# Performance work log

Measured on AMD Instinct MI355X. Metric: run time of the kernel, lower is better.

The kernel has to match this reference:

```python
import jax, jax.numpy as jnp
import numpy as np

N_NODES = 100000


def gcn_layer(x, W, b, src, dst, n):
    # PyG GCNConv: h = x @ W, then D^{-1/2}(A+I)D^{-1/2} aggregation, then + b
    h = x @ W  # [N, out]
    ones = jnp.ones(src.shape[0], dtype=h.dtype)
    deg = jax.ops.segment_sum(ones, dst, num_segments=n) + 1.0  # +1 for self loop
    dinv = jax.lax.rsqrt(deg)  # [N]
    norm = dinv[src] * dinv[dst]  # [E]
    msgs = h[src] * norm[:, None]  # gather + scale, [E, out]
    agg = jax.ops.segment_sum(msgs, dst, num_segments=n)
    agg = agg + h * (dinv * dinv)[:, None]  # self-loop term
    return agg + b


def setup_inputs() -> dict:
    key = jax.random.key(0)
    k1, k2, k3, k4, k5, k6 = jax.random.split(key, 6)
    in_dim, h1, h2 = 256, 128, 64
    x = jax.random.normal(k1, (N_NODES, in_dim), dtype=jnp.float32)
    edge_index = jax.random.randint(k2, (2, 1600000), 0, N_NODES, dtype=jnp.int64)
    # Glorot-style init for weights, zeros for bias (PyG default)
    W1 = jax.random.normal(k3, (in_dim, h1), dtype=jnp.float32) / np.sqrt(in_dim)
    b1 = jnp.zeros((h1,), dtype=jnp.float32)
    W2 = jax.random.normal(k4, (h1, h2), dtype=jnp.float32) / np.sqrt(h1)
    b2 = jnp.zeros((h2,), dtype=jnp.float32)
    return {"x": x, "W1": W1, "b1": b1, "W2": W2, "b2": b2, "edge_index": edge_index}


def reference(x, W1, b1, W2, b2, edge_index):
    src, dst = edge_index[0], edge_index[1]
    n = x.shape[0]
    h = jax.nn.relu(gcn_layer(x, W1, b1, src, dst, n))
    h = jax.nn.relu(gcn_layer(h, W2, b2, src, dst, n))
    return h
```

## Files before the change

### kernel.cpp

```cpp
#include <hip/hip_runtime.h>
#include <hip/hip_bf16.h>


typedef __attribute__((ext_vector_type(8))) short bf16x8;
typedef __attribute__((ext_vector_type(4))) float f32x4;

__device__ inline unsigned short f2bf(float f) {
    unsigned u = __float_as_uint(f);
    u = (u + 0x7fff + ((u >> 16) & 1)) >> 16;
    return (unsigned short)u;
}
__device__ inline float bf2f(unsigned short h) {
    return __uint_as_float(((unsigned)h) << 16);
}
__device__ inline float bflo(unsigned u) { return __uint_as_float(u << 16); }
__device__ inline float bfhi(unsigned u) { return __uint_as_float(u & 0xffff0000u); }
__device__ inline unsigned pack_bf16_2(float lo, float hi) {
    return (unsigned)f2bf(lo) | ((unsigned)f2bf(hi) << 16);
}
__device__ inline void cvt8(const float* v, bf16x8& h8, bf16x8& l8) {
    #pragma unroll
    for (int j = 0; j < 8; ++j) {
        unsigned short h = f2bf(v[j]);
        h8[j] = (short)h;
        l8[j] = (short)f2bf(v[j] - bf2f(h));
    }
}

__global__ void prep_kernel(const int* __restrict__ dst, int* __restrict__ deg, int E,
        const float* __restrict__ W1, unsigned short* __restrict__ w1h,
        unsigned short* __restrict__ w1l,
        const float* __restrict__ W2, unsigned short* __restrict__ w2h,
        unsigned short* __restrict__ w2l) {
    const int W1B = (256 * 128) / 256;
    const int W2B = (128 * 64) / 256;
    int b = blockIdx.x;
    if (b < W1B) {
        int idx = b * 256 + threadIdx.x;
        int k = idx >> 7, n = idx & 127;
        float v = W1[idx];
        unsigned short h = f2bf(v);
        w1h[(size_t)n * 256 + k] = h;
        w1l[(size_t)n * 256 + k] = f2bf(v - bf2f(h));
    } else if (b < W1B + W2B) {
        int idx = (b - W1B) * 256 + threadIdx.x;
        int k = idx >> 6, n = idx & 63;
        float v = W2[idx];
        unsigned short h = f2bf(v);
        w2h[(size_t)n * 128 + k] = h;
        w2l[(size_t)n * 128 + k] = f2bf(v - bf2f(h));
    } else {
        int nb = gridDim.x - (W1B + W2B);
        int stride = nb * 256;
        for (int i = (b - W1B - W2B) * 256 + threadIdx.x; i < E; i += stride)
            atomicAdd(&deg[dst[i]], 1);
    }
}

__global__ __launch_bounds__(1024) void scan_partial_kernel(const int* __restrict__ deg,
        int* __restrict__ psum, float* __restrict__ dinv, int n) {
    __shared__ int wsum[16];
    int tid = threadIdx.x, wave = tid >> 6, lane = tid & 63;
    int i0 = blockIdx.x * 4096 + tid * 4;
    int v0 = 0, v1 = 0, v2 = 0, v3 = 0;
    if (i0 + 3 < n) {
        int4 v = *(const int4*)(deg + i0);
        v0 = v.x; v1 = v.y; v2 = v.z; v3 = v.w;
    } else {
        if (i0 + 0 < n) v0 = deg[i0 + 0];
        if (i0 + 1 < n) v1 = deg[i0 + 1];
        if (i0 + 2 < n) v2 = deg[i0 + 2];
        if (i0 + 3 < n) v3 = deg[i0 + 3];
    }
    if (i0 + 0 < n) dinv[i0 + 0] = 1.0f / sqrtf((float)v0 + 1.0f);
    if (i0 + 1 < n) dinv[i0 + 1] = 1.0f / sqrtf((float)v1 + 1.0f);
    if (i0 + 2 < n) dinv[i0 + 2] = 1.0f / sqrtf((float)v2 + 1.0f);
    if (i0 + 3 < n) dinv[i0 + 3] = 1.0f / sqrtf((float)v3 + 1.0f);
    int s = v0 + v1 + v2 + v3;
    #pragma unroll
    for (int off = 1; off < 64; off <<= 1) s += __shfl_xor(s, off, 64);
    if (lane == 0) wsum[wave] = s;
    __syncthreads();
    if (tid == 0) {
        int t = 0;
        #pragma unroll
        for (int w = 0; w < 16; ++w) t += wsum[w];
        psum[blockIdx.x] = t;
    }
}

__global__ __launch_bounds__(1024) void scan_local_kernel(const int* __restrict__ deg,
        const int* __restrict__ psum, int* __restrict__ offs, int n, int sb) {
    __shared__ int wsum[16];
    int tid = threadIdx.x, wave = tid >> 6, lane = tid & 63;
    int bid = blockIdx.x;
    int base = 0, total = 0;
    for (int w = 0; w < sb; ++w) {
        int t = psum[w];
        if (w < bid) base += t;
        total += t;
    }
    if (bid == 0 && tid == 0) offs[n] = total;

    int i0 = bid * 4096 + tid * 4;
    int v0 = 0, v1 = 0, v2 = 0, v3 = 0;
    if (i0 + 3 < n) {
        int4 v = *(const int4*)(deg + i0);
        v0 = v.x; v1 = v.y; v2 = v.z; v3 = v.w;
    } else {
        if (i0 + 0 < n) v0 = deg[i0 + 0];
        if (i0 + 1 < n) v1 = deg[i0 + 1];
        if (i0 + 2 < n) v2 = deg[i0 + 2];
        if (i0 + 3 < n) v3 = deg[i0 + 3];
    }
    int s = v0 + v1 + v2 + v3;
    int x = s;
    #pragma unroll
    for (int off = 1; off < 64; off <<= 1) {
        int y = __shfl_up(x, off, 64);
        if (lane >= off) x += y;
    }
    if (lane == 63) wsum[wave] = x;
    __syncthreads();
    int wbase = 0;
    #pragma unroll
    for (int w = 0; w < 16; ++w)
        if (w < wave) wbase += wsum[w];
    int ex = base + wbase + (x - s);
    if (i0 + 0 < n) offs[i0 + 0] = ex;
    if (i0 + 1 < n) offs[i0 + 1] = ex + v0;
    if (i0 + 2 < n) offs[i0 + 2] = ex + v0 + v1;
    if (i0 + 3 < n) offs[i0 + 3] = ex + v0 + v1 + v2;
}

__global__ void fill_kernel(const int* __restrict__ src, const int* __restrict__ dst,
        const int* __restrict__ offs, int* __restrict__ cursor,
        int* __restrict__ csr, int E) {
    int stride = gridDim.x * blockDim.x;
    for (int i = blockIdx.x * blockDim.x + threadIdx.x; i < E; i += stride) {
        int d = dst[i];
        int pos = offs[d] + atomicAdd(&cursor[d], 1);
        csr[pos] = src[i];
    }
}

__global__ __launch_bounds__(256) void gemm1_kernel(const float* __restrict__ X,
        const unsigned short* __restrict__ Wh, const unsigned short* __restrict__ Wl,
        const float* __restrict__ dinv, unsigned short* __restrict__ G, int M) {
    constexpr int K = 256;
    const int tid = threadIdx.x;
    const int wv = tid >> 6, ln = tid & 63;
    const int l16 = ln & 15, kseg = ln >> 4;
    const int wr = wv >> 1, wc = wv & 1;
    const int r0 = blockIdx.x * 64 + wr * 32;

    int rA0 = r0 + l16;       if (rA0 >= M) rA0 = M - 1;
    int rA1 = r0 + 16 + l16;  if (rA1 >= M) rA1 = M - 1;
    const float* pA0 = X + (size_t)rA0 * K + kseg * 8;
    const float* pA1 = X + (size_t)rA1 * K + kseg * 8;

    f32x4 acc[2][4];
    #pragma unroll
    for (int a = 0; a < 2; ++a)
        #pragma unroll
        for (int b = 0; b < 4; ++b) acc[a][b] = 0;

    float4 qa0 = *(const float4*)(pA0);
    float4 qb0 = *(const float4*)(pA0 + 4);
    float4 qa1 = *(const float4*)(pA1);
    float4 qb1 = *(const float4*)(pA1 + 4);

    #pragma unroll 2
    for (int k0 = 0; k0 < K; k0 += 32) {
        bf16x8 ah[2], al[2];
        {
            float v[8] = {qa0.x, qa0.y, qa0.z, qa0.w, qb0.x, qb0.y, qb0.z, qb0.w};
            cvt8(v, ah[0], al[0]);
        }
        {
            float v[8] = {qa1.x, qa1.y, qa1.z, qa1.w, qb1.x, qb1.y, qb1.z, qb1.w};
            cvt8(v, ah[1], al[1]);
        }
        if (k0 + 32 < K) {
            qa0 = *(const float4*)(pA0 + k0 + 32);
            qb0 = *(const float4*)(pA0 + k0 + 36);
            qa1 = *(const float4*)(pA1 + k0 + 32);
            qb1 = *(const float4*)(pA1 + k0 + 36);
        }
        #pragma unroll
        for (int tc = 0; tc < 4; ++tc) {
            size_t wo = (size_t)(wc * 64 + tc * 16 + l16) * K + k0 + kseg * 8;
            bf16x8 bh = *(const bf16x8*)(Wh + wo);
            bf16x8 bl = *(const bf16x8*)(Wl + wo);
            #pragma unroll
            for (int tr = 0; tr < 2; ++tr) {
                acc[tr][tc] = __builtin_amdgcn_mfma_f32_16x16x32_bf16(ah[tr], bh, acc[tr][tc], 0, 0, 0);
                acc[tr][tc] = __builtin_amdgcn_mfma_f32_16x16x32_bf16(al[tr], bh, acc[tr][tc], 0, 0, 0);
                acc[tr][tc] = __builtin_amdgcn_mfma_f32_16x16x32_bf16(ah[tr], bl, acc[tr][tc], 0, 0, 0);
            }
        }
    }

    #pragma unroll
    for (int tr = 0; tr < 2; ++tr) {
        int rbase = r0 + tr * 16 + (ln >> 4) * 4;
        #pragma unroll
        for (int r = 0; r < 4; ++r) {
            int row = rbase + r;
            if (row < M) {
                float dv = dinv[row];
                #pragma unroll
                for (int tc = 0; tc < 4; ++tc)
                    G[(size_t)row * 128 + wc * 64 + tc * 16 + l16] =
                        f2bf(acc[tr][tc][r] * dv);
            }
        }
    }
}

__global__ __launch_bounds__(256) void gemm2_kernel(const unsigned short* __restrict__ H,
        const unsigned short* __restrict__ Wh, const unsigned short* __restrict__ Wl,
        const float* __restrict__ dinv, unsigned short* __restrict__ G, int M) {
    constexpr int K = 128;
    const int tid = threadIdx.x;
    const int wv = tid >> 6, ln = tid & 63;
    const int l16 = ln & 15, kseg = ln >> 4;
    const int r0 = blockIdx.x * 64 + wv * 16;

    int rA0 = r0 + l16;  if (rA0 >= M) rA0 = M - 1;
    const unsigned short* pA0 = H + (size_t)rA0 * K + kseg * 8;

    f32x4 acc[4];
    #pragma unroll
    for (int b = 0; b < 4; ++b) acc[b] = 0;

    #pragma unroll
    for (int k0 = 0; k0 < K; k0 += 32) {
        bf16x8 a0 = *(const bf16x8*)(pA0 + k0);
        #pragma unroll
        for (int tc = 0; tc < 4; ++tc) {
            size_t wo = (size_t)(tc * 16 + l16) * K + k0 + kseg * 8;
            bf16x8 bh = *(const bf16x8*)(Wh + wo);
            bf16x8 bl = *(const bf16x8*)(Wl + wo);
            acc[tc] = __builtin_amdgcn_mfma_f32_16x16x32_bf16(a0, bh, acc[tc], 0, 0, 0);
            acc[tc] = __builtin_amdgcn_mfma_f32_16x16x32_bf16(a0, bl, acc[tc], 0, 0, 0);
        }
    }

    {
        int rbase = r0 + (ln >> 4) * 4;
        #pragma unroll
        for (int r = 0; r < 4; ++r) {
            int row = rbase + r;
            if (row < M) {
                float dv = dinv[row];
                #pragma unroll
                for (int tc = 0; tc < 4; ++tc)
                    G[(size_t)row * 64 + tc * 16 + l16] = f2bf(acc[tc][r] * dv);
            }
        }
    }
}

__global__ __launch_bounds__(256) void aggregate128_kernel(const unsigned* __restrict__ G,
        const int* __restrict__ csr, const int* __restrict__ offs,
        const float* __restrict__ dinv, const float* __restrict__ bias,
        unsigned* __restrict__ out, int n) {
    int wave = threadIdx.x >> 6, lane = threadIdx.x & 63;
    int node = blockIdx.x * 4 + wave;
    if (node >= n) return;
    int beg = offs[node], end = offs[node + 1];

    unsigned u = G[(size_t)node * 64 + lane];
    float a0 = bflo(u), a1 = bfhi(u);
    int e = beg;
    for (; e + 8 <= end; e += 8) {
        unsigned uu[8];
        #pragma unroll
        for (int j = 0; j < 8; ++j) uu[j] = G[(size_t)csr[e + j] * 64 + lane];
        #pragma unroll
        for (int j = 0; j < 8; ++j) { a0 += bflo(uu[j]); a1 += bfhi(uu[j]); }
    }
    for (; e + 4 <= end; e += 4) {
        unsigned uu[4];
        #pragma unroll
        for (int j = 0; j < 4; ++j) uu[j] = G[(size_t)csr[e + j] * 64 + lane];
        #pragma unroll
        for (int j = 0; j < 4; ++j) { a0 += bflo(uu[j]); a1 += bfhi(uu[j]); }
    }
    for (; e < end; ++e) {
        unsigned u0 = G[(size_t)csr[e] * 64 + lane];
        a0 += bflo(u0);
        a1 += bfhi(u0);
    }
    float di = dinv[node];
    float rx = fmaxf(fmaf(a0, di, bias[lane * 2 + 0]), 0.0f);
    float ry = fmaxf(fmaf(a1, di, bias[lane * 2 + 1]), 0.0f);
    out[(size_t)node * 64 + lane] = pack_bf16_2(rx, ry);
}

__global__ __launch_bounds__(256) void aggregate64_kernel(const unsigned* __restrict__ G,
        const int* __restrict__ csr, const int* __restrict__ offs,
        const float* __restrict__ dinv, const float* __restrict__ bias,
        float* __restrict__ out, int n) {
    int wave = threadIdx.x >> 6, lane = threadIdx.x & 63;
    int node = blockIdx.x * 4 + wave;
    if (node >= n) return;
    int beg = offs[node], end = offs[node + 1];
    int half = lane >> 5, col = lane & 31;

    float a0 = 0.0f, a1 = 0.0f;
    if (half == 0) {
        unsigned u = G[(size_t)node * 32 + col];
        a0 = bflo(u); a1 = bfhi(u);
    }
    int e = beg;
    for (; e + 8 <= end; e += 8) {
        unsigned uu[4];
        #pragma unroll
        for (int j = 0; j < 4; ++j) uu[j] = G[(size_t)csr[e + 2 * j + half] * 32 + col];
        #pragma unroll
        for (int j = 0; j < 4; ++j) { a0 += bflo(uu[j]); a1 += bfhi(uu[j]); }
    }
    for (; e + 2 <= end; e += 2) {
        unsigned uA = G[(size_t)csr[e + half] * 32 + col];
        a0 += bflo(uA);
        a1 += bfhi(uA);
    }
    if (e < end && half == 0) {
        unsigned uA = G[(size_t)csr[e] * 32 + col];
        a0 += bflo(uA);
        a1 += bfhi(uA);
    }
    a0 += __shfl_down(a0, 32, 64);
    a1 += __shfl_down(a1, 32, 64);
    if (half == 0) {
        float di = dinv[node];
        float2 r;
        r.x = fmaxf(fmaf(a0, di, bias[col * 2 + 0]), 0.0f);
        r.y = fmaxf(fmaf(a1, di, bias[col * 2 + 1]), 0.0f);
        ((float2*)(out + (size_t)node * 64))[col] = r;
    }
}

extern "C" void kernel_launch(void* const* d_in, const int* in_sizes, int n_in,
                              void* d_out, int out_size, void* d_ws, size_t ws_size,
                              hipStream_t stream) {
    const float* x  = (const float*)d_in[0];
    const float* W1 = (const float*)d_in[1];
    const float* b1 = (const float*)d_in[2];
    const float* W2 = (const float*)d_in[3];
    const float* b2 = (const float*)d_in[4];
    const int* edge = (const int*)d_in[5];

    const int IN = 256, H1 = 128, H2 = 64;
    const int E = in_sizes[5] / 2;
    const int N = in_sizes[0] / IN;
    const int* srcp = edge;
    const int* dstp = edge + E;

    char* ws = (char*)d_ws;
    auto alignup = [](size_t v) { return (v + 255) & ~(size_t)255; };
    size_t off = 0;
    size_t degSz = alignup((size_t)N * 4);
    int*            deg    = (int*)(ws + off);            off += degSz;
    int*            cursor = (int*)(ws + off);            off += degSz;
    int*            offs   = (int*)(ws + off);            off += alignup(((size_t)N + 1) * 4);
    float*          dinv   = (float*)(ws + off);          off += degSz;
    int*            psum   = (int*)(ws + off);            off += alignup(64 * 4);
    int*            csr    = (int*)(ws + off);            off += alignup((size_t)E * 4);
    unsigned short* wt1h   = (unsigned short*)(ws + off); off += alignup((size_t)IN * H1 * 2);
    unsigned short* wt1l   = (unsigned short*)(ws + off); off += alignup((size_t)IN * H1 * 2);
    unsigned short* wt2h   = (unsigned short*)(ws + off); off += alignup((size_t)H1 * H2 * 2);
    unsigned short* wt2l   = (unsigned short*)(ws + off); off += alignup((size_t)H1 * H2 * 2);
    unsigned short* g1     = (unsigned short*)(ws + off); off += alignup((size_t)N * H1 * 2);
    unsigned*       h1b    = (unsigned*)(ws + off);       off += alignup((size_t)N * (H1 / 2) * 4);
    unsigned short* g2     = g1;

    hipMemsetAsync(deg, 0, 2 * degSz, stream);

    int sb = (N + 4095) / 4096;

    prep_kernel<<<160 + 2048, 256, 0, stream>>>(dstp, deg, E, W1, wt1h, wt1l,
                                                W2, wt2h, wt2l);
    scan_partial_kernel<<<sb, 1024, 0, stream>>>(deg, psum, dinv, N);
    scan_local_kernel<<<sb, 1024, 0, stream>>>(deg, psum, offs, N, sb);
    fill_kernel<<<1024, 256, 0, stream>>>(srcp, dstp, offs, cursor, csr, E);

    int g64 = (N + 63) / 64;
    int agrid = (N + 3) / 4;

    gemm1_kernel<<<g64, 256, 0, stream>>>(x, wt1h, wt1l, dinv, g1, N);
    aggregate128_kernel<<<agrid, 256, 0, stream>>>((const unsigned*)g1, csr, offs,
                                                   dinv, b1, h1b, N);
    gemm2_kernel<<<g64, 256, 0, stream>>>((const unsigned short*)h1b, wt2h, wt2l,
                                          dinv, g2, N);
    aggregate64_kernel<<<agrid, 256, 0, stream>>>((const unsigned*)g2, csr, offs,
                                                  dinv, b2, (float*)d_out, N);
}
```

Measured before the change: 534.1 us.

## Stage GEMM weights in LDS, enlarge tiles, use packed bf16 conversion

Both GEMM kernels now load the full hi/lo bf16 weight matrices into shared memory once per 1024-thread block. They read B fragments from LDS instead of reloading them from global memory on every tile. Blocks cover 256 or 512 rows with 4 row tiles per wave, so each weight fragment is reused across more rows. The fp32-to-bf16 hi/lo split in gemm1 now uses the hardware v_cvt_pk_bf16_f32 instruction instead of manual rounding. The risks are heavy LDS use (128KB for gemm1), which limits occupancy, and the loss of the software prefetch of X in gemm1.

```diff
diff --git a/kernel.cpp b/kernel.cpp
--- a/kernel.cpp
+++ b/kernel.cpp
@@ -18,13 +18,20 @@
 __device__ inline unsigned pack_bf16_2(float lo, float hi) {
     return (unsigned)f2bf(lo) | ((unsigned)f2bf(hi) << 16);
 }
-__device__ inline void cvt8(const float* v, bf16x8& h8, bf16x8& l8) {
-    #pragma unroll
-    for (int j = 0; j < 8; ++j) {
-        unsigned short h = f2bf(v[j]);
-        h8[j] = (short)h;
-        l8[j] = (short)f2bf(v[j] - bf2f(h));
-    }
+__device__ inline unsigned cvtpk(float a, float b) {
+    unsigned r;
+    asm("v_cvt_pk_bf16_f32 %0, %1, %2" : "=v"(r) : "v"(a), "v"(b));
+    return r;
+}
+__device__ inline void split8(float4 qa, float4 qb, bf16x8& h8, bf16x8& l8) {
+    float v0=qa.x, v1=qa.y, v2=qa.z, v3=qa.w, v4=qb.x, v5=qb.y, v6=qb.z, v7=qb.w;
+    unsigned h0=cvtpk(v0,v1), h1=cvtpk(v2,v3), h2=cvtpk(v4,v5), h3=cvtpk(v6,v7);
+    float r0=v0-bflo(h0), r1=v1-bfhi(h0), r2=v2-bflo(h1), r3=v3-bfhi(h1);
+    float r4=v4-bflo(h2), r5=v5-bfhi(h2), r6=v6-bflo(h3), r7=v7-bfhi(h3);
+    unsigned l0=cvtpk(r0,r1), l1=cvtpk(r2,r3), l2=cvtpk(r4,r5), l3=cvtpk(r6,r7);
+    uint4 H = make_uint4(h0,h1,h2,h3), L = make_uint4(l0,l1,l2,l3);
+    h8 = __builtin_bit_cast(bf16x8, H);
+    l8 = __builtin_bit_cast(bf16x8, L);
 }
 
 __global__ void prep_kernel(const int* __restrict__ dst, int* __restrict__ deg, int E,
@@ -144,65 +151,70 @@
     }
 }
 
-__global__ __launch_bounds__(256) void gemm1_kernel(const float* __restrict__ X,
+__global__ __launch_bounds__(1024, 4) void gemm1_kernel(const float* __restrict__ X,
         const unsigned short* __restrict__ Wh, const unsigned short* __restrict__ Wl,
         const float* __restrict__ dinv, unsigned short* __restrict__ G, int M) {
-    constexpr int K = 256;
+    __shared__ uint4 LH[4096];
+    __shared__ uint4 LL[4096];
     const int tid = threadIdx.x;
+    {
+        const uint4* gh = (const uint4*)Wh;
+        const uint4* gl = (const uint4*)Wl;
+        #pragma unroll
+        for (int j = 0; j < 4; ++j) {
+            int i = tid + j * 1024;
+            int kb = i >> 7, n = i & 127;
+            LH[i] = gh[n * 32 + kb];
+            LL[i] = gl[n * 32 + kb];
+        }
+    }
+    __syncthreads();
+
     const int wv = tid >> 6, ln = tid & 63;
     const int l16 = ln & 15, kseg = ln >> 4;
-    const int wr = wv >> 1, wc = wv & 1;
-    const int r0 = blockIdx.x * 64 + wr * 32;
-
-    int rA0 = r0 + l16;       if (rA0 >= M) rA0 = M - 1;
-    int rA1 = r0 + 16 + l16;  if (rA1 >= M) rA1 = M - 1;
-    const float* pA0 = X + (size_t)rA0 * K + kseg * 8;
-    const float* pA1 = X + (size_t)rA1 * K + kseg * 8;
-
-    f32x4 acc[2][4];
-    #pragma unroll
-    for (int a = 0; a < 2; ++a)
-        #pragma unroll
-        for (int b = 0; b < 4; ++b) acc[a][b] = 0;
-
-    float4 qa0 = *(const float4*)(pA0);
-    float4 qb0 = *(const float4*)(pA0 + 4);
-    float4 qa1 = *(const float4*)(pA1);
-    float4 qb1 = *(const float4*)(pA1 + 4);
-
-    #pragma unroll 2
-    for (int k0 = 0; k0 < K; k0 += 32) {
-        bf16x8 ah[2], al[2];
-        {
-            float v[8] = {qa0.x, qa0.y, qa0.z, qa0.w, qb0.x, qb0.y, qb0.z, qb0.w};
-            cvt8(v, ah[0], al[0]);
-        }
-        {
-            float v[8] = {qa1.x, qa1.y, qa1.z, qa1.w, qb1.x, qb1.y, qb1.z, qb1.w};
-            cvt8(v, ah[1], al[1]);
-        }
-        if (k0 + 32 < K) {
-            qa0 = *(const float4*)(pA0 + k0 + 32);
-            qb0 = *(const float4*)(pA0 + k0 + 36);
-            qa1 = *(const float4*)(pA1 + k0 + 32);
-            qb1 = *(const float4*)(pA1 + k0 + 36);
-        }
-        #pragma unroll
-        for (int tc = 0; tc < 4; ++tc) {
-            size_t wo = (size_t)(wc * 64 + tc * 16 + l16) * K + k0 + kseg * 8;
-            bf16x8 bh = *(const bf16x8*)(Wh + wo);
-            bf16x8 bl = *(const bf16x8*)(Wl + wo);
+    const int wr = wv >> 2, wc = wv & 3;
+    const int r0 = blockIdx.x * 256 + wr * 64;
+
+    const float* pA[4];
+    #pragma unroll
+    for (int tr = 0; tr < 4; ++tr) {
+        int rr = r0 + tr * 16 + l16;
+        if (rr >= M) rr = M - 1;
+        pA[tr] = X + (size_t)rr * 256 + kseg * 8;
+    }
+
+    f32x4 acc[4][2];
+    #pragma unroll
+    for (int a = 0; a < 4; ++a)
+        #pragma unroll
+        for (int b = 0; b < 2; ++b) acc[a][b] = 0;
+
+    for (int k0 = 0; k0 < 256; k0 += 32) {
+        const int kb4 = (k0 >> 3) + kseg;
+        bf16x8 bh[2], bl[2];
+        #pragma unroll
+        for (int tc = 0; tc < 2; ++tc) {
+            int li = kb4 * 128 + wc * 32 + tc * 16 + l16;
+            bh[tc] = __builtin_bit_cast(bf16x8, LH[li]);
+            bl[tc] = __builtin_bit_cast(bf16x8, LL[li]);
+        }
+        #pragma unroll
+        for (int tr = 0; tr < 4; ++tr) {
+            float4 qa = *(const float4*)(pA[tr] + k0);
+            float4 qb = *(const float4*)(pA[tr] + k0 + 4);
+            bf16x8 ah, al;
+            split8(qa, qb, ah, al);
             #pragma unroll
-            for (int tr = 0; tr < 2; ++tr) {
-                acc[tr][tc] = __builtin_amdgcn_mfma_f32_16x16x32_bf16(ah[tr], bh, acc[tr][tc], 0, 0, 0);
-                acc[tr][tc] = __builtin_amdgcn_mfma_f32_16x16x32_bf16(al[tr], bh, acc[tr][tc], 0, 0, 0);
-                acc[tr][tc] = __builtin_amdgcn_mfma_f32_16x16x32_bf16(ah[tr], bl, acc[tr][tc], 0, 0, 0);
+            for (int tc = 0; tc < 2; ++tc) {
+                acc[tr][tc] = __builtin_amdgcn_mfma_f32_16x16x32_bf16(ah, bh[tc], acc[tr][tc], 0, 0, 0);
+                acc[tr][tc] = __builtin_amdgcn_mfma_f32_16x16x32_bf16(al, bh[tc], acc[tr][tc], 0, 0, 0);
+                acc[tr][tc] = __builtin_amdgcn_mfma_f32_16x16x32_bf16(ah, bl[tc], acc[tr][tc], 0, 0, 0);
             }
         }
     }
 
     #pragma unroll
-    for (int tr = 0; tr < 2; ++tr) {
+    for (int tr = 0; tr < 4; ++tr) {
         int rbase = r0 + tr * 16 + (ln >> 4) * 4;
         #pragma unroll
         for (int r = 0; r < 4; ++r) {
@@ -210,53 +222,78 @@
             if (row < M) {
                 float dv = dinv[row];
                 #pragma unroll
-                for (int tc = 0; tc < 4; ++tc)
-                    G[(size_t)row * 128 + wc * 64 + tc * 16 + l16] =
+                for (int tc = 0; tc < 2; ++tc)
+                    G[(size_t)row * 128 + wc * 32 + tc * 16 + l16] =
                         f2bf(acc[tr][tc][r] * dv);
             }
         }
     }
 }
 
-__global__ __launch_bounds__(256) void gemm2_kernel(const unsigned short* __restrict__ H,
+__global__ __launch_bounds__(1024, 4) void gemm2_kernel(const unsigned short* __restrict__ H,
         const unsigned short* __restrict__ Wh, const unsigned short* __restrict__ Wl,
         const float* __restrict__ dinv, unsigned short* __restrict__ G, int M) {
-    constexpr int K = 128;
+    __shared__ uint4 LH[1024];
+    __shared__ uint4 LL[1024];
     const int tid = threadIdx.x;
+    {
+        int kb = tid >> 6, n = tid & 63;
+        LH[tid] = ((const uint4*)Wh)[n * 16 + kb];
+        LL[tid] = ((const uint4*)Wl)[n * 16 + kb];
+    }
+    __syncthreads();
+
     const int wv = tid >> 6, ln = tid & 63;
     const int l16 = ln & 15, kseg = ln >> 4;
-    const int r0 = blockIdx.x * 64 + wv * 16;
-
-    int rA0 = r0 + l16;  if (rA0 >= M) rA0 = M - 1;
-    const unsigned short* pA0 = H + (size_t)rA0 * K + kseg * 8;
-
-    f32x4 acc[4];
-    #pragma unroll
-    for (int b = 0; b < 4; ++b) acc[b] = 0;
-
-    #pragma unroll
-    for (int k0 = 0; k0 < K; k0 += 32) {
-        bf16x8 a0 = *(const bf16x8*)(pA0 + k0);
-        #pragma unroll
-        for (int tc = 0; tc < 4; ++tc) {
-            size_t wo = (size_t)(tc * 16 + l16) * K + k0 + kseg * 8;
-            bf16x8 bh = *(const bf16x8*)(Wh + wo);
-            bf16x8 bl = *(const bf16x8*)(Wl + wo);
-            acc[tc] = __builtin_amdgcn_mfma_f32_16x16x32_bf16(a0, bh, acc[tc], 0, 0, 0);
-            acc[tc] = __builtin_amdgcn_mfma_f32_16x16x32_bf16(a0, bl, acc[tc], 0, 0, 0);
-        }
-    }
-
-    {
-        int rbase = r0 + (ln >> 4) * 4;
+    const int wr = wv >> 1, wc = wv & 1;
+    const int r0 = blockIdx.x * 512 + wr * 64;
+
+    const unsigned short* pA[4];
+    #pragma unroll
+    for (int tr = 0; tr < 4; ++tr) {
+        int rr = r0 + tr * 16 + l16;
+        if (rr >= M) rr = M - 1;
+        pA[tr] = H + (size_t)rr * 128 + kseg * 8;
+    }
+
+    f32x4 acc[4][2];
+    #pragma unroll
+    for (int a = 0; a < 4; ++a)
+        #pragma unroll
+        for (int b = 0; b < 2; ++b) acc[a][b] = 0;
+
+    for (int k0 = 0; k0 < 128; k0 += 32) {
+        const int kb4 = (k0 >> 3) + kseg;
+        bf16x8 bh[2], bl[2];
+        #pragma unroll
+        for (int tc = 0; tc < 2; ++tc) {
+            int li = kb4 * 64 + wc * 32 + tc * 16 + l16;
+            bh[tc] = __builtin_bit_cast(bf16x8, LH[li]);
+            bl[tc] = __builtin_bit_cast(bf16x8, LL[li]);
+        }
+        #pragma unroll
+        for (int tr = 0; tr < 4; ++tr) {
+            bf16x8 a0 = *(const bf16x8*)(pA[tr] + k0);
+            #pragma unroll
+            for (int tc = 0; tc < 2; ++tc) {
+                acc[tr][tc] = __builtin_amdgcn_mfma_f32_16x16x32_bf16(a0, bh[tc], acc[tr][tc], 0, 0, 0);
+                acc[tr][tc] = __builtin_amdgcn_mfma_f32_16x16x32_bf16(a0, bl[tc], acc[tr][tc], 0, 0, 0);
+            }
+        }
+    }
+
+    #pragma unroll
+    for (int tr = 0; tr < 4; ++tr) {
+        int rbase = r0 + tr * 16 + (ln >> 4) * 4;
         #pragma unroll
         for (int r = 0; r < 4; ++r) {
             int row = rbase + r;
             if (row < M) {
                 float dv = dinv[row];
                 #pragma unroll
-                for (int tc = 0; tc < 4; ++tc)
-                    G[(size_t)row * 64 + tc * 16 + l16] = f2bf(acc[tc][r] * dv);
+                for (int tc = 0; tc < 2; ++tc)
+                    G[(size_t)row * 64 + wc * 32 + tc * 16 + l16] =
+                        f2bf(acc[tr][tc][r] * dv);
             }
         }
     }
@@ -387,14 +424,15 @@
     scan_local_kernel<<<sb, 1024, 0, stream>>>(deg, psum, offs, N, sb);
     fill_kernel<<<1024, 256, 0, stream>>>(srcp, dstp, offs, cursor, csr, E);
 
-    int g64 = (N + 63) / 64;
-    int agrid = (N + 3) / 4;
-
-    gemm1_kernel<<<g64, 256, 0, stream>>>(x, wt1h, wt1l, dinv, g1, N);
+    int g1grid = (N + 255) / 256;
+    int g2grid = (N + 511) / 512;
+    int agrid  = (N + 3) / 4;
+
+    gemm1_kernel<<<g1grid, 1024, 0, stream>>>(x, wt1h, wt1l, dinv, g1, N);
     aggregate128_kernel<<<agrid, 256, 0, stream>>>((const unsigned*)g1, csr, offs,
                                                    dinv, b1, h1b, N);
-    gemm2_kernel<<<g64, 256, 0, stream>>>((const unsigned short*)h1b, wt2h, wt2l,
-                                          dinv, g2, N);
+    gemm2_kernel<<<g2grid, 1024, 0, stream>>>((const unsigned short*)h1b, wt2h, wt2l,
+                                              dinv, g2, N);
     aggregate64_kernel<<<agrid, 256, 0, stream>>>((const unsigned*)g2, csr, offs,
                                                   dinv, b2, (float*)d_out, N);
 }
```

Measured after the change: 495.0 us. 7.3% less time.
